# Performance work log

Measured on AMD Instinct MI355X. Metric: run time of the kernel, lower is better.

The kernel has to match this reference:

```python
import jax, jax.numpy as jnp
import numpy as np

D = 100  # hidden dim: kernel has 3*D = 300 entries (concat(a, b, a*b))


def setup_inputs() -> dict:
    key = jax.random.key(0)
    k1, k2, k3 = jax.random.split(key, 3)
    context = jax.random.normal(k1, (16384, D), dtype=jnp.float32)
    question = jax.random.normal(k2, (4096, D), dtype=jnp.float32)
    kernel = jax.random.normal(k3, (3 * D,), dtype=jnp.float32)
    return {"context": context, "question": question, "kernel": kernel}


def reference(context, question, kernel):
    # kernel . concat(a, b, a*b) = a.w1 + b.w2 + (a*b).w3, computed without
    # materializing the [N, M, 3D] feature tensor.
    w1, w2, w3 = kernel[:D], kernel[D:2 * D], kernel[2 * D:]
    # S: [N, M] similarity matrix
    S = (context @ w1)[:, None] + (question @ w2)[None, :] \
        + (context * w3) @ question.T
    # C2Q: row-softmax over question positions, weighted sum of question
    A = jax.nn.softmax(S, axis=-1)            # [N, M]
    U_A = A @ question                          # [N, D]
    # Q2C: softmax over per-row maxes, weighted sum of context, tiled to rows
    b = jax.nn.softmax(jnp.max(S, axis=-1))    # [N]
    h = b @ context                             # [D]
    H_A = jnp.broadcast_to(h, context.shape)   # [N, D]
    # megamerge: [N, 4D]
    G = jnp.concatenate([context, U_A, context * U_A, context * H_A], axis=-1)
    return G
```

## Files before the change

kernel.cpp:

```cpp
#include <hip/hip_runtime.h>

typedef _Float16 f16x8 __attribute__((ext_vector_type(8)));
typedef float    f32x4 __attribute__((ext_vector_type(4)));
typedef float    f32x16 __attribute__((ext_vector_type(16)));
typedef unsigned int u32;

#define N_CTX 16384
#define N_Q   4096
#define DIM   100
#define THR   5.7708f
#define LOG2E 1.4426950408889634f
#define LN2   0.6931471805599453f

union FragU { unsigned int u[4]; f16x8 v; };

#if __has_builtin(__builtin_amdgcn_exp2f)
#define EXP2(x) __builtin_amdgcn_exp2f(x)
#else
#define EXP2(x) exp2f(x)
#endif

#define MFMA32(a, b, c) __builtin_amdgcn_mfma_f32_32x32x16_f16((a), (b), (c), 0, 0, 0)
#define GLOAD_LDS(g, l) __builtin_amdgcn_global_load_lds( \
    (const __attribute__((address_space(1))) u32*)(const void*)(g), \
    (__attribute__((address_space(3))) u32*)(void*)(l), 16, 0, 0)

__global__ void prep_all(const float* __restrict__ q, const float* __restrict__ ctx,
                         const float* __restrict__ ker,
                         unsigned short* __restrict__ qbS, unsigned short* __restrict__ qTS,
                         unsigned short* __restrict__ cbH, float* __restrict__ a) {
    int b = blockIdx.x;
    int tid = threadIdx.x;
    if (b < 64) {
        __shared__ _Float16 ldsT[100][64];
        __shared__ float tL[64];
        int j0 = b * 64;
        int r = tid >> 2, c = tid & 3;
        const float* row = q + (size_t)(j0 + r) * DIM + c * 25;
        float part = 0.f;
        #pragma unroll
        for (int k = 0; k < 25; ++k) {
            float v = row[k];
            ldsT[c * 25 + k][r] = (_Float16)v;
            part += v * ker[100 + c * 25 + k];
        }
        part += __shfl_xor(part, 1, 64);
        part += __shfl_xor(part, 2, 64);
        if (c == 0) tL[r] = part * LOG2E;
        __syncthreads();

        #pragma unroll
        for (int k = 0; k < 4; ++k) {
            int ci = tid + k * 256;
            int jb = ci >> 9;
            int rem = ci & 511;
            int dt = rem >> 7, rem2 = rem & 127;
            int o = rem2 >> 5, rr = rem2 & 31;
            int d = dt * 32 + rr;
            f16x8 v;
            #pragma unroll
            for (int e = 0; e < 8; ++e) {
                int jl = jb * 32 + 8 * o + e;
                v[e] = (d < DIM) ? ldsT[d][jl] : (d == DIM ? (_Float16)1.f : (_Float16)0.f);
            }
            char* dst = (char*)qTS + (size_t)((j0 >> 5) + jb) * 8192
                        + dt * 2048 + o * 512 + rr * 16;
            *reinterpret_cast<f16x8*>(dst) = v;
        }

        #pragma unroll
        for (int k = 0; k < 4; ++k) {
            int ci = tid + k * 256;
            int jl = ci & 63;
            int o  = ci >> 6;
            int j5 = jl & 31;
            int g = j5 >> 2, gm = g & 3;
            if (gm == 1 || gm == 2) g ^= 3;
            int slot = (g << 2) | (j5 & 3);
            int img  = (j0 >> 5) + (jl >> 5);
            f16x8 h;
            #pragma unroll
            for (int e = 0; e < 8; ++e) {
                int d = 8 * o + e;
                float v = (d < DIM) ? (float)ldsT[d][jl] * LOG2E
                                    : (d == DIM ? tL[jl] : 0.f);
                h[e] = (_Float16)v;
            }
            *reinterpret_cast<f16x8*>((char*)qbS + (size_t)img * 8192 + o * 512 + slot * 16) = h;
        }
    } else {
        int i = (b - 64) * 256 + tid;
        const float* row = ctx + (size_t)i * DIM;
        float buf[100];
        float acc = 0.f;
        #pragma unroll
        for (int d4 = 0; d4 < 25; ++d4) {
            #pragma unroll
            for (int e = 0; e < 4; ++e) {
                float v = row[4 * d4 + e];
                buf[4 * d4 + e] = v;
                acc += v * ker[4 * d4 + e];
            }
        }
        a[i] = acc;
        unsigned short* orow = cbH + (size_t)i * 128;
        #pragma unroll
        for (int c = 0; c < 16; ++c) {
            f16x8 h;
            #pragma unroll
            for (int e = 0; e < 8; ++e) {
                int d = 8 * c + e;
                float v = (d < DIM) ? buf[d] * ker[200 + d] : (d == DIM ? 1.f : 0.f);
                h[e] = (_Float16)v;
            }
            *reinterpret_cast<f16x8*>(orow + 8 * c) = h;
        }
    }
}

__global__ __launch_bounds__(256, 4) void attn_main(
    const unsigned short* __restrict__ qbS, const unsigned short* __restrict__ qTS,
    const unsigned short* __restrict__ cbH,
    _Float16* __restrict__ Ub, float* __restrict__ mb,
    float* __restrict__ lb, float* __restrict__ mtb)
{
    __shared__ __align__(16) char stageMem[2][16384];

    const int tid  = threadIdx.x;
    const int w    = tid >> 6;
    const int lane = tid & 63;
    const int hi   = lane >> 5;
    const int c31  = lane & 31;
    const int it   = blockIdx.x;
    const int js   = blockIdx.y;
    const int JS   = gridDim.y;
    const int R    = (N_Q / 32) / JS;
    const int iw0  = it * 128 + w * 32;

    f16x8 cbF[7];
    {
        const unsigned short* crow = cbH + (size_t)(iw0 + c31) * 128 + 8 * hi;
        #pragma unroll
        for (int kk = 0; kk < 7; ++kk)
            cbF[kk] = *reinterpret_cast<const f16x8*>(crow + kk * 16);
    }

    f32x16 U0 = {}, U1 = {}, U2 = {}, U3 = {};
    float m = -INFINITY, mtrue = -INFINITY;

    const int bb0 = js * R;
    const int seg = w * 2;
    const int l16 = lane * 16;

    auto stage_fn = [&](int buf, int bb) {
        const char* gq = (const char*)qbS + (size_t)bb * 8192;
        const char* gt = (const char*)qTS + (size_t)bb * 8192;
        char* lq = stageMem[buf];
        #pragma unroll
        for (int k = 0; k < 2; ++k)
            GLOAD_LDS(gq + (seg + k) * 1024 + l16, lq + (seg + k) * 1024);
        #pragma unroll
        for (int k = 0; k < 2; ++k)
            GLOAD_LDS(gt + (seg + k) * 1024 + l16, lq + 8192 + (seg + k) * 1024);
    };

    stage_fn(0, bb0);
    __syncthreads();
    int cur = 0;

    for (int r = 0; r < R; ++r) {
        if (r + 1 < R) stage_fn(cur ^ 1, bb0 + r + 1);

        const char* qbL = stageMem[cur];
        const char* qTL = stageMem[cur] + 8192;

        f32x16 sacc = {};
        __builtin_amdgcn_s_setprio(1);
        #pragma unroll
        for (int kk = 0; kk < 7; ++kk) {
            f16x8 aq = *reinterpret_cast<const f16x8*>(qbL + kk * 1024 + l16);
            sacc = MFMA32(aq, cbF[kk], sacc);
        }
        __builtin_amdgcn_s_setprio(0);

        float sc[16];
        #pragma unroll
        for (int q16 = 0; q16 < 16; ++q16) sc[q16] = sacc[q16];

        float x0 = fmaxf(fmaxf(sc[0],  sc[1]),  sc[2]);
        float x1 = fmaxf(fmaxf(sc[3],  sc[4]),  sc[5]);
        float x2 = fmaxf(fmaxf(sc[6],  sc[7]),  sc[8]);
        float x3 = fmaxf(fmaxf(sc[9],  sc[10]), sc[11]);
        float x4 = fmaxf(fmaxf(sc[12], sc[13]), sc[14]);
        float tm = fmaxf(fmaxf(fmaxf(x0, x1), x2), fmaxf(fmaxf(x3, x4), sc[15]));
        mtrue = fmaxf(mtrue, tm);

        if (__any(tm > m + THR)) {
            float tmf = fmaxf(tm, __shfl_xor(tm, 32, 64));
            float mn = fmaxf(m, tmf);
            float scale = EXP2(m - mn);
            U0 *= scale; U1 *= scale; U2 *= scale; U3 *= scale;
            m = mn;
        }

        #pragma unroll
        for (int q16 = 0; q16 < 16; ++q16) sc[q16] = EXP2(sc[q16] - m);

        FragU f0, f1;
        #pragma unroll
        for (int e2 = 0; e2 < 4; ++e2) {
            auto p0 = __builtin_amdgcn_cvt_pkrtz(sc[2 * e2],     sc[2 * e2 + 1]);
            auto p1 = __builtin_amdgcn_cvt_pkrtz(sc[8 + 2 * e2], sc[8 + 2 * e2 + 1]);
            f0.u[e2] = __builtin_bit_cast(unsigned int, p0);
            f1.u[e2] = __builtin_bit_cast(unsigned int, p1);
        }

        __builtin_amdgcn_s_setprio(1);
        {
            f16x8 a0 = *reinterpret_cast<const f16x8*>(qTL + l16);
            f16x8 a1 = *reinterpret_cast<const f16x8*>(qTL + 1024 + l16);
            U0 = MFMA32(a0, f0.v, U0);
            U0 = MFMA32(a1, f1.v, U0);
        }
        {
            f16x8 a0 = *reinterpret_cast<const f16x8*>(qTL + 2048 + l16);
            f16x8 a1 = *reinterpret_cast<const f16x8*>(qTL + 3072 + l16);
            U1 = MFMA32(a0, f0.v, U1);
            U1 = MFMA32(a1, f1.v, U1);
        }
        {
            f16x8 a0 = *reinterpret_cast<const f16x8*>(qTL + 4096 + l16);
            f16x8 a1 = *reinterpret_cast<const f16x8*>(qTL + 5120 + l16);
            U2 = MFMA32(a0, f0.v, U2);
            U2 = MFMA32(a1, f1.v, U2);
        }
        {
            f16x8 a0 = *reinterpret_cast<const f16x8*>(qTL + 6144 + l16);
            f16x8 a1 = *reinterpret_cast<const f16x8*>(qTL + 7168 + l16);
            U3 = MFMA32(a0, f0.v, U3);
            U3 = MFMA32(a1, f1.v, U3);
        }
        __builtin_amdgcn_s_setprio(0);

        __syncthreads();
        cur ^= 1;
    }

    mtrue = fmaxf(mtrue, __shfl_xor(mtrue, 32, 64));
    float ltmp = __shfl_xor(U3[0], 32, 64);
    float lfull = hi ? U3[0] : ltmp;

    int irow = iw0 + c31;
    if (hi == 0) {
        mb [(size_t)js * N_CTX + irow] = m;
        lb [(size_t)js * N_CTX + irow] = lfull;
        mtb[(size_t)js * N_CTX + irow] = mtrue * LN2;
    }
    _Float16* ub = Ub + (((size_t)js * 128 + it) * DIM) * 128 + w * 32 + c31;
    #pragma unroll
    for (int r = 0; r < 16; ++r) {
        int dl = (r & 3) + 8 * (r >> 2) + 4 * hi;
        ub[(size_t)dl * 128]        = (_Float16)U0[r];
        ub[(size_t)(32 + dl) * 128] = (_Float16)U1[r];
        ub[(size_t)(64 + dl) * 128] = (_Float16)U2[r];
        if (96 + dl < DIM) ub[(size_t)(96 + dl) * 128] = (_Float16)U3[r];
    }
}


template<int JS>
__global__ void kernel_mf(const float* __restrict__ a, const float* __restrict__ mtb,
                          float* __restrict__ mfull) {
    int i = blockIdx.x * 256 + threadIdx.x;
    float mt = -INFINITY;
    #pragma unroll
    for (int js = 0; js < JS; ++js) mt = fmaxf(mt, mtb[(size_t)js * N_CTX + i]);
    mfull[i] = a[i] + mt;
}

__global__ void kernel_h(const float* __restrict__ mfull, const float* __restrict__ ctx,
                         float* __restrict__ hp) {
    __shared__ float sm[256];
    __shared__ float smh[8][104];
    int t = threadIdx.x;
    float v = -INFINITY;
    for (int i = t; i < N_CTX; i += 256) v = fmaxf(v, mfull[i]);
    sm[t] = v; __syncthreads();
    for (int s = 128; s > 0; s >>= 1) { if (t < s) sm[t] = fmaxf(sm[t], sm[t + s]); __syncthreads(); }
    float M = sm[0];
    __syncthreads();
    float z = 0.f;
    for (int i = t; i < N_CTX; i += 256) z += __expf(mfull[i] - M);
    sm[t] = z; __syncthreads();
    for (int s = 128; s > 0; s >>= 1) { if (t < s) sm[t] += sm[t + s]; __syncthreads(); }
    float Z = sm[0];
    __syncthreads();

    int rr = t >> 5, d32 = t & 31;
    int i0 = blockIdx.x * 64;
    float a0 = 0.f, a1 = 0.f, a2 = 0.f, a3 = 0.f;
    for (int g = 0; g < 8; ++g) {
        int row = i0 + g * 8 + rr;
        float bw = __expf(mfull[row] - M);
        const float* cr = ctx + (size_t)row * DIM;
        a0 += bw * cr[d32];
        a1 += bw * cr[d32 + 32];
        a2 += bw * cr[d32 + 64];
        if (d32 < 4) a3 += bw * cr[d32 + 96];
    }
    smh[rr][d32]      = a0;
    smh[rr][d32 + 32] = a1;
    smh[rr][d32 + 64] = a2;
    if (d32 < 4) smh[rr][d32 + 96] = a3;
    __syncthreads();
    if (t < DIM) {
        float s = 0.f;
        #pragma unroll
        for (int g = 0; g < 8; ++g) s += smh[g][t];
        hp[blockIdx.x * 128 + t] = s / Z;
    }
}

template<int JS>
__global__ __launch_bounds__(256, 4) void combine(
    const _Float16* __restrict__ Ub, const float* __restrict__ mb,
    const float* __restrict__ lb, const float* __restrict__ hp,
    const float* __restrict__ ctx, float* __restrict__ G)
{
    __shared__ __align__(16) float ctxL[32][100];
    __shared__ __align__(16) float uaL[32][100];
    __shared__ __align__(16) float hL[100];

    const int b   = blockIdx.x;
    const int tid = threadIdx.x;

    for (int idx = tid; idx < 800; idx += 256) {
        int r = idx / 25, c4 = idx - r * 25;
        *reinterpret_cast<f32x4*>(&ctxL[r][c4 * 4]) =
            *reinterpret_cast<const f32x4*>(ctx + (size_t)(b * 32 + r) * DIM + c4 * 4);
    }
    if (tid < DIM) {
        float s = 0.f;
        for (int bb = 0; bb < 256; ++bb) s += hp[bb * 128 + tid];
        hL[tid] = s;
    }
    __syncthreads();

    {
        int i32 = tid & 31, seg = tid >> 5;
        int row = b * 32 + i32;
        int iblk = row >> 7, il = row & 127;
        float mw[JS];
        float M = -INFINITY;
        #pragma unroll
        for (int js = 0; js < JS; ++js) {
            mw[js] = mb[(size_t)js * N_CTX + row];
            M = fmaxf(M, mw[js]);
        }
        float ew[JS];
        float L = 0.f;
        #pragma unroll
        for (int js = 0; js < JS; ++js) {
            ew[js] = EXP2(mw[js] - M);
            L += lb[(size_t)js * N_CTX + row] * ew[js];
        }
        float invL = 1.f / L;
        for (int d = seg; d < DIM; d += 8) {
            float u = 0.f;
            #pragma unroll
            for (int js = 0; js < JS; ++js)
                u += (float)Ub[(((size_t)js * 128 + iblk) * DIM + d) * 128 + il] * ew[js];
            uaL[i32][d] = u * invL;
        }
    }
    __syncthreads();

    float* gOut = G + (size_t)b * 32 * 400;
    for (int idx = tid; idx < 3200; idx += 256) {
        int r = idx / 100, c4 = idx - r * 100;
        int sel = c4 / 25, d4 = (c4 - sel * 25) * 4;
        f32x4 cv = *reinterpret_cast<const f32x4*>(&ctxL[r][d4]);
        f32x4 out;
        if (sel == 0)      out = cv;
        else if (sel == 1) out = *reinterpret_cast<const f32x4*>(&uaL[r][d4]);
        else if (sel == 2) out = *reinterpret_cast<const f32x4*>(&uaL[r][d4]) * cv;
        else               out = cv * *reinterpret_cast<const f32x4*>(&hL[d4]);
        *reinterpret_cast<f32x4*>(gOut + (size_t)r * 400 + c4 * 4) = out;
    }
}

extern "C" void kernel_launch(void* const* d_in, const int* in_sizes, int n_in,
                              void* d_out, int out_size, void* d_ws, size_t ws_size,
                              hipStream_t stream) {
    const float* ctx = (const float*)d_in[0];
    const float* q   = (const float*)d_in[1];
    const float* ker = (const float*)d_in[2];
    float* G = (float*)d_out;

    char* ws = (char*)d_ws;
    unsigned short* qbS   = (unsigned short*)(ws);
    unsigned short* qTS   = (unsigned short*)(ws + 1048576);
    unsigned short* cbH   = (unsigned short*)(ws + 2097152);
    float*          a     = (float*)(ws + 6291456);
    float*          mfull = (float*)(ws + 6356992);
    float*          hp    = (float*)(ws + 6422528);
    const size_t fixed = 6554112;

    int JS = 8;
    if (fixed + 8ull * 3473408ull > ws_size) JS = 4;
    if (fixed + 4ull * 3473408ull > ws_size) JS = 2;

    _Float16* Ub  = (_Float16*)(ws + fixed);
    size_t ubB    = (size_t)JS * 3276800ull;
    float*    mb  = (float*)(ws + fixed + ubB);
    float*    lb  = (float*)(ws + fixed + ubB + (size_t)JS * 65536ull);
    float*    mtb = (float*)(ws + fixed + ubB + (size_t)JS * 131072ull);

    prep_all<<<dim3(128), dim3(256), 0, stream>>>(q, ctx, ker, qbS, qTS, cbH, a);
    attn_main<<<dim3(128, JS), dim3(256), 0, stream>>>(qbS, qTS, cbH, Ub, mb, lb, mtb);

    if (JS == 8) {
        kernel_mf<8><<<dim3(64), dim3(256), 0, stream>>>(a, mtb, mfull);
        kernel_h<<<dim3(256), dim3(256), 0, stream>>>(mfull, ctx, hp);
        combine<8><<<dim3(512), dim3(256), 0, stream>>>(Ub, mb, lb, hp, ctx, G);
    } else if (JS == 4) {
        kernel_mf<4><<<dim3(64), dim3(256), 0, stream>>>(a, mtb, mfull);
        kernel_h<<<dim3(256), dim3(256), 0, stream>>>(mfull, ctx, hp);
        combine<4><<<dim3(512), dim3(256), 0, stream>>>(Ub, mb, lb, hp, ctx, G);
    } else {
        kernel_mf<2><<<dim3(64), dim3(256), 0, stream>>>(a, mtb, mfull);
        kernel_h<<<dim3(256), dim3(256), 0, stream>>>(mfull, ctx, hp);
        combine<2><<<dim3(512), dim3(256), 0, stream>>>(Ub, mb, lb, hp, ctx, G);
    }
}
```

Measured before the change: 96.64 us.

## Hierarchical max/sum for Q2C softmax instead of redundant per-block full scans

Previously each of 256 kernel_h blocks rescanned all 16384 row maxima twice to compute the global max and normalizer. Now kernel_mf produces per-block partial maxima, kernel_h reads only those 64 partials, accumulates the exponent sum alongside the weighted context sum, and uses 64 blocks over 256 rows each. The final normalization moves into combine, which sums 64 partial h vectors and partial Z values. This removes redundant global reads and reductions, at the cost of fewer blocks in kernel_h and a few extra partial buffers in the workspace.

```diff
diff --git a/kernel.cpp b/kernel.cpp
--- a/kernel.cpp
+++ b/kernel.cpp
@@ -270,36 +270,34 @@
 
 template<int JS>
 __global__ void kernel_mf(const float* __restrict__ a, const float* __restrict__ mtb,
-                          float* __restrict__ mfull) {
-    int i = blockIdx.x * 256 + threadIdx.x;
+                          float* __restrict__ mfull, float* __restrict__ Mp) {
+    __shared__ float sm[256];
+    int t = threadIdx.x;
+    int i = blockIdx.x * 256 + t;
     float mt = -INFINITY;
     #pragma unroll
     for (int js = 0; js < JS; ++js) mt = fmaxf(mt, mtb[(size_t)js * N_CTX + i]);
-    mfull[i] = a[i] + mt;
-}
-
-__global__ void kernel_h(const float* __restrict__ mfull, const float* __restrict__ ctx,
-                         float* __restrict__ hp) {
-    __shared__ float sm[256];
-    __shared__ float smh[8][104];
-    int t = threadIdx.x;
-    float v = -INFINITY;
-    for (int i = t; i < N_CTX; i += 256) v = fmaxf(v, mfull[i]);
+    float v = a[i] + mt;
+    mfull[i] = v;
     sm[t] = v; __syncthreads();
     for (int s = 128; s > 0; s >>= 1) { if (t < s) sm[t] = fmaxf(sm[t], sm[t + s]); __syncthreads(); }
-    float M = sm[0];
-    __syncthreads();
-    float z = 0.f;
-    for (int i = t; i < N_CTX; i += 256) z += __expf(mfull[i] - M);
-    sm[t] = z; __syncthreads();
-    for (int s = 128; s > 0; s >>= 1) { if (t < s) sm[t] += sm[t + s]; __syncthreads(); }
-    float Z = sm[0];
-    __syncthreads();
+    if (t == 0) Mp[blockIdx.x] = sm[0];
+}
+
+__global__ void kernel_h(const float* __restrict__ mfull, const float* __restrict__ Mp,
+                         const float* __restrict__ ctx,
+                         float* __restrict__ hp, float* __restrict__ zp) {
+    __shared__ float smh[8][104];
+    __shared__ float smz[8];
+    int t = threadIdx.x;
+    float M = -INFINITY;
+    #pragma unroll 8
+    for (int k = 0; k < 64; ++k) M = fmaxf(M, Mp[k]);
 
     int rr = t >> 5, d32 = t & 31;
-    int i0 = blockIdx.x * 64;
-    float a0 = 0.f, a1 = 0.f, a2 = 0.f, a3 = 0.f;
-    for (int g = 0; g < 8; ++g) {
+    int i0 = blockIdx.x * 256;
+    float a0 = 0.f, a1 = 0.f, a2 = 0.f, a3 = 0.f, wz = 0.f;
+    for (int g = 0; g < 32; ++g) {
         int row = i0 + g * 8 + rr;
         float bw = __expf(mfull[row] - M);
         const float* cr = ctx + (size_t)row * DIM;
@@ -307,17 +305,25 @@
         a1 += bw * cr[d32 + 32];
         a2 += bw * cr[d32 + 64];
         if (d32 < 4) a3 += bw * cr[d32 + 96];
+        wz += bw;
     }
     smh[rr][d32]      = a0;
     smh[rr][d32 + 32] = a1;
     smh[rr][d32 + 64] = a2;
     if (d32 < 4) smh[rr][d32 + 96] = a3;
+    if (d32 == 0) smz[rr] = wz;
     __syncthreads();
     if (t < DIM) {
         float s = 0.f;
         #pragma unroll
         for (int g = 0; g < 8; ++g) s += smh[g][t];
-        hp[blockIdx.x * 128 + t] = s / Z;
+        hp[blockIdx.x * DIM + t] = s;
+    }
+    if (t == 0) {
+        float z = 0.f;
+        #pragma unroll
+        for (int g = 0; g < 8; ++g) z += smz[g];
+        zp[blockIdx.x] = z;
     }
 }
 
@@ -325,7 +331,8 @@
 __global__ __launch_bounds__(256, 4) void combine(
     const _Float16* __restrict__ Ub, const float* __restrict__ mb,
     const float* __restrict__ lb, const float* __restrict__ hp,
-    const float* __restrict__ ctx, float* __restrict__ G)
+    const float* __restrict__ zp, const float* __restrict__ ctx,
+    float* __restrict__ G)
 {
     __shared__ __align__(16) float ctxL[32][100];
     __shared__ __align__(16) float uaL[32][100];
@@ -340,9 +347,10 @@
             *reinterpret_cast<const f32x4*>(ctx + (size_t)(b * 32 + r) * DIM + c4 * 4);
     }
     if (tid < DIM) {
-        float s = 0.f;
-        for (int bb = 0; bb < 256; ++bb) s += hp[bb * 128 + tid];
-        hL[tid] = s;
+        float s = 0.f, z = 0.f;
+        #pragma unroll 8
+        for (int bb = 0; bb < 64; ++bb) { s += hp[bb * DIM + tid]; z += zp[bb]; }
+        hL[tid] = s / z;
     }
     __syncthreads();
 
@@ -404,6 +412,8 @@
     float*          a     = (float*)(ws + 6291456);
     float*          mfull = (float*)(ws + 6356992);
     float*          hp    = (float*)(ws + 6422528);
+    float*          zp    = (float*)(ws + 6448128);
+    float*          Mp    = (float*)(ws + 6448384);
     const size_t fixed = 6554112;
 
     int JS = 8;
@@ -420,16 +430,16 @@
     attn_main<<<dim3(128, JS), dim3(256), 0, stream>>>(qbS, qTS, cbH, Ub, mb, lb, mtb);
 
     if (JS == 8) {
-        kernel_mf<8><<<dim3(64), dim3(256), 0, stream>>>(a, mtb, mfull);
-        kernel_h<<<dim3(256), dim3(256), 0, stream>>>(mfull, ctx, hp);
-        combine<8><<<dim3(512), dim3(256), 0, stream>>>(Ub, mb, lb, hp, ctx, G);
+        kernel_mf<8><<<dim3(64), dim3(256), 0, stream>>>(a, mtb, mfull, Mp);
+        kernel_h<<<dim3(64), dim3(256), 0, stream>>>(mfull, Mp, ctx, hp, zp);
+        combine<8><<<dim3(512), dim3(256), 0, stream>>>(Ub, mb, lb, hp, zp, ctx, G);
     } else if (JS == 4) {
-        kernel_mf<4><<<dim3(64), dim3(256), 0, stream>>>(a, mtb, mfull);
-        kernel_h<<<dim3(256), dim3(256), 0, stream>>>(mfull, ctx, hp);
-        combine<4><<<dim3(512), dim3(256), 0, stream>>>(Ub, mb, lb, hp, ctx, G);
+        kernel_mf<4><<<dim3(64), dim3(256), 0, stream>>>(a, mtb, mfull, Mp);
+        kernel_h<<<dim3(64), dim3(256), 0, stream>>>(mfull, Mp, ctx, hp, zp);
+        combine<4><<<dim3(512), dim3(256), 0, stream>>>(Ub, mb, lb, hp, zp, ctx, G);
     } else {
-        kernel_mf<2><<<dim3(64), dim3(256), 0, stream>>>(a, mtb, mfull);
-        kernel_h<<<dim3(256), dim3(256), 0, stream>>>(mfull, ctx, hp);
-        combine<2><<<dim3(512), dim3(256), 0, stream>>>(Ub, mb, lb, hp, ctx, G);
-    }
-}
+        kernel_mf<2><<<dim3(64), dim3(256), 0, stream>>>(a, mtb, mfull, Mp);
+        kernel_h<<<dim3(64), dim3(256), 0, stream>>>(mfull, Mp, ctx, hp, zp);
+        combine<2><<<dim3(512), dim3(256), 0, stream>>>(Ub, mb, lb, hp, zp, ctx, G);
+    }
+}
```

New measurement: 89.21 us, median of 2. 7.7% less time.
